# Kernel optimization log

Measured on AMD Instinct MI355X. Metric: run time of the kernel, lower is better.

The kernel has to match this reference:

```python
import jax, jax.numpy as jnp
import numpy as np

HEADS = 8
DIM_HEAD = 64
C = 512              # in_channels == inner_dim = heads*dim_head
WIN = 7              # window size implied by rel_pos table (2*7-1 = 13)
EPS = 1e-5


def setup_inputs() -> dict:
    key = jax.random.key(0)
    ks = jax.random.split(key, 6)
    B = 2048
    inner = HEADS * DIM_HEAD
    x = jax.random.normal(ks[0], (B, C, WIN, WIN), dtype=jnp.float32)
    gamma = jnp.ones((C,), dtype=jnp.float32)
    beta = jnp.zeros((C,), dtype=jnp.float32)
    w_qkv = jax.random.normal(ks[1], (C, 3 * inner), dtype=jnp.float32) / np.sqrt(C)
    rel_table = jax.random.normal(ks[2], (2 * WIN - 1, 2 * WIN - 1, HEADS), dtype=jnp.float32)
    w_out = jax.random.normal(ks[3], (inner, C), dtype=jnp.float32) / np.sqrt(inner)
    b_out = jnp.zeros((C,), dtype=jnp.float32)
    return {"x": x, "gamma": gamma, "beta": beta, "w_qkv": w_qkv,
            "rel_table": rel_table, "w_out": w_out, "b_out": b_out}


def _rel_pos_bias(rel_table, H, W):
    # Swin-style additive bias: bias[h, i, j] = table[hi-hj+H-1, wi-wj+W-1, h]
    hh = jnp.arange(H)
    ww = jnp.arange(W)
    hi = jnp.repeat(hh, W)          # [N] row index of each flattened position
    wi = jnp.tile(ww, H)            # [N] col index
    dh = hi[:, None] - hi[None, :] + (H - 1)   # [N, N]
    dw = wi[:, None] - wi[None, :] + (W - 1)   # [N, N]
    bias = rel_table[dh, dw]        # [N, N, heads]
    return jnp.transpose(bias, (2, 0, 1))      # [heads, N, N]


def reference(x, gamma, beta, w_qkv, rel_table, w_out, b_out):
    B, Cc, H, W = x.shape
    N = H * W
    shortcut = x
    xs = jnp.transpose(x.reshape(B, Cc, N), (0, 2, 1))   # [B, N, C]
    # LayerNorm over channel dim
    mu = jnp.mean(xs, axis=-1, keepdims=True)
    var = jnp.var(xs, axis=-1, keepdims=True)
    xn = (xs - mu) * jax.lax.rsqrt(var + EPS) * gamma + beta
    qkv = xn @ w_qkv                                      # [B, N, 3*inner]
    q, k, v = jnp.split(qkv, 3, axis=-1)
    def heads(t):
        return jnp.transpose(t.reshape(B, N, HEADS, DIM_HEAD), (0, 2, 1, 3))  # [B,h,N,d]
    q, k, v = heads(q), heads(k), heads(v)
    scale = DIM_HEAD ** -0.5
    dots = jnp.einsum('bhnd,bhmd->bhnm', q, k) * scale   # [B,h,N,N]
    dots = dots + _rel_pos_bias(rel_table, H, W)[None]   # add Swin-style bias
    attn = jax.nn.softmax(dots, axis=-1)
    out = jnp.einsum('bhnm,bhmd->bhnd', attn, v)         # [B,h,N,d]
    out = jnp.transpose(out, (0, 2, 1, 3)).reshape(B, N, HEADS * DIM_HEAD)
    out = out @ w_out + b_out                            # [B, N, C]
    out = jnp.transpose(out, (0, 2, 1)).reshape(B, Cc, H, W)
    return out + shortcut
```

## Files before the change

### kernel.cpp

```cpp
#include <hip/hip_runtime.h>

#define BATCH 2048
#define CH 512
#define NTOK 49
#define NHEAD 8
#define DHEAD 64

typedef __attribute__((ext_vector_type(8))) short bf16x8;
typedef __attribute__((ext_vector_type(4))) float f32x4;

__device__ __forceinline__ ushort f2bf(float f) {
  union { float f; unsigned u; } v; v.f = f;
  unsigned r = v.u + 0x7fffu + ((v.u >> 16) & 1u);
  return (ushort)(r >> 16);
}

__device__ __forceinline__ float bf2f(ushort u) {
  union { unsigned u; float f; } v; v.u = ((unsigned)u) << 16;
  return v.f;
}

#define MFMA16(a, b, c) __builtin_amdgcn_mfma_f32_16x16x32_bf16((a), (b), (c), 0, 0, 0)

#define GLOAD_LDS16(gsrc, ldst)                                                  \
  __builtin_amdgcn_global_load_lds((const __attribute__((address_space(1))) void*)(gsrc), \
                                   (__attribute__((address_space(3))) void*)(ldst), 16, 0, 0)

__global__ void prep_kernel(const float* __restrict__ w_qkv, const float* __restrict__ w_out,
                            const float* __restrict__ rel, ushort* __restrict__ wqkvB,
                            ushort* __restrict__ woutF, float* __restrict__ biasP) {
  int tid = blockIdx.x * blockDim.x + threadIdx.x;
  int stride = gridDim.x * blockDim.x;
  for (int i = tid; i < 12 * 16 * 8 * 64 * 8; i += stride) {
    int j = i & 7, lane = (i >> 3) & 63, cbs = (i >> 9) & 7, kk = (i >> 12) & 15, nb = i >> 16;
    int o = nb * 128 + cbs * 16 + (lane & 15);
    int c = kk * 32 + (lane >> 4) * 8 + j;
    wqkvB[i] = f2bf(w_qkv[c * 1536 + o]);
  }
  for (int i = tid; i < 32 * 16 * 64 * 8; i += stride) {
    int j = i & 7, lane = (i >> 3) & 63, ks = (i >> 9) & 15, cb = i >> 13;
    int o = cb * 16 + (lane & 15);
    int c = ks * 32 + (lane >> 4) * 8 + j;
    woutF[i] = f2bf(w_out[c * 512 + o]);
  }
  for (int i = tid; i < NHEAD * 64 * 64; i += stride) {
    int h = i >> 12, n = (i >> 6) & 63, m = i & 63;
    float v = -1e30f;
    if (n < NTOK && m < NTOK) {
      int dh = n / 7 - m / 7 + 6;
      int dw = n % 7 - m % 7 + 6;
      v = rel[(dh * 13 + dw) * 8 + h];
    }
    biasP[i] = v;
  }
}

__global__ __launch_bounds__(256) void ln_kernel(const float* __restrict__ x,
                                                 const float* __restrict__ gamma,
                                                 const float* __restrict__ beta,
                                                 ushort* __restrict__ xnW) {
  int b = blockIdx.x;
  int t = threadIdx.x;
  __shared__ ushort xsb[CH][NTOK];
  __shared__ float muL[64], rsL[64];
  const float4* x4 = (const float4*)(x + (size_t)b * CH * NTOK);
  for (int i4 = t; i4 < CH * NTOK / 4; i4 += 256) {
    float4 v = x4[i4];
    int lf = i4 * 4;
#pragma unroll
    for (int e = 0; e < 4; e++) {
      int idx = lf + e;
      int c = idx / NTOK, n = idx - c * NTOK;
      xsb[c][n] = f2bf(((const float*)&v)[e]);
    }
  }
  __syncthreads();
  int row = t >> 2, sub = t & 3;
  float s = 0.f, s2 = 0.f;
  if (row < NTOK) {
    for (int c = sub; c < CH; c += 4) {
      float v = bf2f(xsb[c][row]);
      s += v;
      s2 += v * v;
    }
  }
  s += __shfl_xor(s, 1);
  s += __shfl_xor(s, 2);
  s2 += __shfl_xor(s2, 1);
  s2 += __shfl_xor(s2, 2);
  if (sub == 0 && row < NTOK) {
    float m = s * (1.f / CH);
    muL[row] = m;
    rsL[row] = rsqrtf(s2 * (1.f / CH) - m * m + 1e-5f);
  }
  __syncthreads();
  ushort* dst = xnW + (size_t)b * NTOK * CH;
  for (int i = t; i < NTOK * 64; i += 256) {
    int n = i >> 6, c0 = (i & 63) * 8;
    float mu = muL[n], rs = rsL[n];
    ushort tmp[8];
#pragma unroll
    for (int j = 0; j < 8; j++) {
      int c = c0 + j;
      tmp[j] = f2bf((bf2f(xsb[c][n]) - mu) * rs * gamma[c] + beta[c]);
    }
    *(uint4*)(dst + (size_t)n * CH + c0) = *(const uint4*)tmp;
  }
}

__global__ __launch_bounds__(256, 4) void qkv_gemm(const ushort* __restrict__ xnW,
                                                   const ushort* __restrict__ wqkvB,
                                                   ushort* __restrict__ qW,
                                                   ushort* __restrict__ kW,
                                                   ushort* __restrict__ vW) {
  int bid = blockIdx.x;
  int f = (bid & 7) * 1536 + (bid >> 3);
  int mb = f / 12, nb = f - mb * 12;
  int b0 = mb * 2;
  int t = threadIdx.x, lane = t & 63, w = t >> 6;
  int wm = w >> 1, wn = w & 1;

  __shared__ __align__(16) ushort lds[8704];

  for (int i = t; i < 2 * 30 * 32; i += 256) {
    int buf = i >= 960;
    int r2 = i - buf * 960;
    int rr = r2 >> 5;
    int row = (rr < 15) ? (49 + rr) : (98 + rr);
    lds[buf * 4096 + row * 32 + (i & 31)] = 0;
  }

  const int arow = lane & 15, g = lane >> 4;
  int srow0 = w * 16 + (lane >> 2);
  int cL = lane & 3;
  const ushort* wBbase = wqkvB + (size_t)nb * 16 * 4096;

  {
#pragma unroll
    for (int i = 0; i < 2; i++) {
      int row = i * 64 + srow0;
      int n = row & 63, bb = b0 + (row >> 6);
      int cG = cL ^ ((row >> 1) & 3);
      if (n < NTOK)
        GLOAD_LDS16(xnW + ((size_t)bb * NTOK + n) * CH + cG * 8, lds + (i * 64 + w * 16) * 32);
    }
  }
  __syncthreads();

  f32x4 acc[4][4];
#pragma unroll
  for (int mt = 0; mt < 4; mt++)
#pragma unroll
    for (int nt = 0; nt < 4; nt++) acc[mt][nt] = (f32x4){0.f, 0.f, 0.f, 0.f};

  int cur = 0;
  for (int step = 0; step < 16; ++step) {
    const ushort* wp = wBbase + (size_t)step * 4096 + (wn * 4) * 512 + lane * 8;
    bf16x8 bfr[4];
#pragma unroll
    for (int nt = 0; nt < 4; nt++) bfr[nt] = *(const bf16x8*)(wp + nt * 512);
    if (step < 15) {
      int nxt = cur ^ 1, kk = step + 1;
#pragma unroll
      for (int i = 0; i < 2; i++) {
        int row = i * 64 + srow0;
        int n = row & 63, bb = b0 + (row >> 6);
        int cG = cL ^ ((row >> 1) & 3);
        if (n < NTOK)
          GLOAD_LDS16(xnW + ((size_t)bb * NTOK + n) * CH + kk * 32 + cG * 8,
                      lds + nxt * 4096 + (i * 64 + w * 16) * 32);
      }
    }
    const ushort* lA = lds + cur * 4096;
    bf16x8 afr[4];
#pragma unroll
    for (int mt = 0; mt < 4; mt++) {
      int row = wm * 64 + mt * 16 + arow;
      afr[mt] = *(const bf16x8*)&lA[row * 32 + (g ^ ((row >> 1) & 3)) * 8];
    }
#pragma unroll
    for (int mt = 0; mt < 4; mt++)
#pragma unroll
      for (int nt = 0; nt < 4; nt++) acc[mt][nt] = MFMA16(afr[mt], bfr[nt], acc[mt][nt]);
    __syncthreads();
    cur ^= 1;
  }

  ushort(*oL)[136] = (ushort(*)[136])lds;
  int h0 = (nb & 3) * 2;
  int sct = nb >> 2;
#pragma unroll
  for (int hh = 0; hh < 2; hh++) {
    if (wm == hh) {
#pragma unroll
      for (int mt = 0; mt < 4; mt++)
#pragma unroll
        for (int nt = 0; nt < 4; nt++)
#pragma unroll
          for (int r = 0; r < 4; r++) {
            int rn = mt * 16 + 4 * g + r;
            oL[rn][wn * 64 + nt * 16 + arow] = f2bf(acc[mt][nt][r]);
          }
    }
    __syncthreads();
    int b = b0 + hh;
    if (sct < 2) {
      ushort* dst = (sct == 0 ? qW : kW);
      for (int i = t; i < NTOK * 16; i += 256) {
        int n = i >> 4, c8 = i & 15;
        int h = h0 + (c8 >> 3);
        *(uint4*)(dst + (size_t)(b * 8 + h) * (NTOK * 64) + n * 64 + (c8 & 7) * 8) =
            *(const uint4*)&oL[n][c8 * 8];
      }
    } else {
      for (int i = t; i < 128 * 8; i += 256) {
        int col = i >> 3, n8 = i & 7;
        int h = h0 + (col >> 6), d = col & 63;
        ushort tmp[8];
#pragma unroll
        for (int jj = 0; jj < 8; jj++) tmp[jj] = oL[n8 * 8 + jj][col];
        *(uint4*)(vW + (size_t)(b * 8 + h) * 4096 + d * 64 + n8 * 8) = *(const uint4*)tmp;
      }
    }
    __syncthreads();
  }
}

__global__ __launch_bounds__(512, 4) void attn2(const ushort* __restrict__ qW,
                                                const ushort* __restrict__ kW,
                                                const ushort* __restrict__ vW,
                                                const float* __restrict__ biasP,
                                                ushort* __restrict__ aoW) {
  int b = blockIdx.x;
  int t = threadIdx.x;
  int lane = t & 63;
  int h = t >> 6;

  __shared__ ushort pL[8][64][72];
  ushort(*pl)[72] = pL[h];

  const int c = lane & 15, g = lane >> 4;
  const ushort* qb = qW + (size_t)(b * 8 + h) * NTOK * 64;
  const ushort* kb = kW + (size_t)(b * 8 + h) * NTOK * 64;
  const ushort* vb = vW + (size_t)(b * 8 + h) * 64 * 64;
  const float* bp = biasP + h * 64 * 64;

  f32x4 s[4][4];
#pragma unroll
  for (int mt = 0; mt < 4; mt++)
#pragma unroll
    for (int nt = 0; nt < 4; nt++) s[mt][nt] = (f32x4){0.f, 0.f, 0.f, 0.f};
#pragma unroll
  for (int ks = 0; ks < 2; ks++) {
    bf16x8 kf[4];
#pragma unroll
    for (int nt = 0; nt < 4; nt++)
      kf[nt] = *(const bf16x8*)(kb + (size_t)(nt * 16 + c) * 64 + ks * 32 + g * 8);
#pragma unroll
    for (int mt = 0; mt < 4; mt++) {
      bf16x8 qf = *(const bf16x8*)(qb + (size_t)(mt * 16 + c) * 64 + ks * 32 + g * 8);
#pragma unroll
      for (int nt = 0; nt < 4; nt++) s[mt][nt] = MFMA16(qf, kf[nt], s[mt][nt]);
    }
  }
#pragma unroll
  for (int mt = 0; mt < 4; mt++)
#pragma unroll
    for (int nt = 0; nt < 4; nt++)
#pragma unroll
      for (int r = 0; r < 4; r++) {
        int n = mt * 16 + 4 * g + r;
        int m = nt * 16 + c;
        s[mt][nt][r] = s[mt][nt][r] * 0.125f + bp[n * 64 + m];
      }

#pragma unroll
  for (int mt = 0; mt < 4; mt++)
#pragma unroll
    for (int r = 0; r < 4; r++) {
      float mx = fmaxf(fmaxf(s[mt][0][r], s[mt][1][r]), fmaxf(s[mt][2][r], s[mt][3][r]));
      mx = fmaxf(mx, __shfl_xor(mx, 1));
      mx = fmaxf(mx, __shfl_xor(mx, 2));
      mx = fmaxf(mx, __shfl_xor(mx, 4));
      mx = fmaxf(mx, __shfl_xor(mx, 8));
      float p0 = __expf(s[mt][0][r] - mx);
      float p1 = __expf(s[mt][1][r] - mx);
      float p2 = __expf(s[mt][2][r] - mx);
      float p3 = __expf(s[mt][3][r] - mx);
      float sum = p0 + p1 + p2 + p3;
      sum += __shfl_xor(sum, 1);
      sum += __shfl_xor(sum, 2);
      sum += __shfl_xor(sum, 4);
      sum += __shfl_xor(sum, 8);
      float rinv = 1.f / sum;
      int n = mt * 16 + 4 * g + r;
      pl[n][0 * 16 + c] = f2bf(p0 * rinv);
      pl[n][1 * 16 + c] = f2bf(p1 * rinv);
      pl[n][2 * 16 + c] = f2bf(p2 * rinv);
      pl[n][3 * 16 + c] = f2bf(p3 * rinv);
    }

  f32x4 o[4][4];
#pragma unroll
  for (int mt = 0; mt < 4; mt++)
#pragma unroll
    for (int nt = 0; nt < 4; nt++) o[mt][nt] = (f32x4){0.f, 0.f, 0.f, 0.f};
#pragma unroll
  for (int ks = 0; ks < 2; ks++) {
    bf16x8 vf[4];
#pragma unroll
    for (int nt = 0; nt < 4; nt++)
      vf[nt] = *(const bf16x8*)(vb + (size_t)(nt * 16 + c) * 64 + ks * 32 + g * 8);
#pragma unroll
    for (int mt = 0; mt < 4; mt++) {
      bf16x8 pf = *(const bf16x8*)&pl[mt * 16 + c][ks * 32 + g * 8];
#pragma unroll
      for (int nt = 0; nt < 4; nt++) o[mt][nt] = MFMA16(pf, vf[nt], o[mt][nt]);
    }
  }

#pragma unroll
  for (int mt = 0; mt < 4; mt++)
#pragma unroll
    for (int nt = 0; nt < 4; nt++)
#pragma unroll
      for (int r = 0; r < 4; r++) {
        int n = mt * 16 + 4 * g + r;
        pl[n][nt * 16 + c] = f2bf(o[mt][nt][r]);
      }
  ushort* ao = aoW + (size_t)b * NTOK * CH + h * 64;
  for (int i = lane; i < NTOK * 8; i += 64) {
    int row = i >> 3, c8 = i & 7;
    *(uint4*)(ao + (size_t)row * CH + c8 * 8) = *(const uint4*)&pl[row][c8 * 8];
  }
}

__global__ __launch_bounds__(256, 4) void proj_kernel(const ushort* __restrict__ aoW,
                                                      const ushort* __restrict__ woutF,
                                                      const float* __restrict__ b_out,
                                                      const float* __restrict__ x,
                                                      float* __restrict__ out) {
  int bid = blockIdx.x;
  int f = (bid & 7) * 512 + (bid >> 3);
  int mb = f >> 2, nbp = f & 3;
  int b0 = mb * 2;
  int t = threadIdx.x, lane = t & 63, w = t >> 6;
  int wm = w >> 1, wn = w & 1;

  __shared__ __align__(16) char ldsraw[33792];
  ushort* lds = (ushort*)ldsraw;
  float(*oL)[132] = (float(*)[132])ldsraw;

  for (int i = t; i < 2 * 30 * 32; i += 256) {
    int buf = i >= 960;
    int r2 = i - buf * 960;
    int rr = r2 >> 5;
    int row = (rr < 15) ? (49 + rr) : (98 + rr);
    lds[buf * 4096 + row * 32 + (i & 31)] = 0;
  }

  const int arow = lane & 15, g = lane >> 4;
  int srow0 = w * 16 + (lane >> 2);
  int cL = lane & 3;

  {
#pragma unroll
    for (int i = 0; i < 2; i++) {
      int row = i * 64 + srow0;
      int n = row & 63, bb = b0 + (row >> 6);
      int cG = cL ^ ((row >> 1) & 3);
      if (n < NTOK)
        GLOAD_LDS16(aoW + ((size_t)bb * NTOK + n) * CH + cG * 8, lds + (i * 64 + w * 16) * 32);
    }
  }
  __syncthreads();

  f32x4 acc[4][4];
#pragma unroll
  for (int mt = 0; mt < 4; mt++)
#pragma unroll
    for (int nt = 0; nt < 4; nt++) acc[mt][nt] = (f32x4){0.f, 0.f, 0.f, 0.f};

  int cur = 0;
  for (int step = 0; step < 16; ++step) {
    const ushort* wp = woutF + ((size_t)(nbp * 8 + wn * 4) * 16 + step) * 512 + lane * 8;
    bf16x8 bfr[4];
#pragma unroll
    for (int nt = 0; nt < 4; nt++) bfr[nt] = *(const bf16x8*)(wp + (size_t)nt * 16 * 512);
    if (step < 15) {
      int nxt = cur ^ 1, kk = step + 1;
#pragma unroll
      for (int i = 0; i < 2; i++) {
        int row = i * 64 + srow0;
        int n = row & 63, bb = b0 + (row >> 6);
        int cG = cL ^ ((row >> 1) & 3);
        if (n < NTOK)
          GLOAD_LDS16(aoW + ((size_t)bb * NTOK + n) * CH + kk * 32 + cG * 8,
                      lds + nxt * 4096 + (i * 64 + w * 16) * 32);
      }
    }
    const ushort* lA = lds + cur * 4096;
    bf16x8 afr[4];
#pragma unroll
    for (int mt = 0; mt < 4; mt++) {
      int row = wm * 64 + mt * 16 + arow;
      afr[mt] = *(const bf16x8*)&lA[row * 32 + (g ^ ((row >> 1) & 3)) * 8];
    }
#pragma unroll
    for (int mt = 0; mt < 4; mt++)
#pragma unroll
      for (int nt = 0; nt < 4; nt++) acc[mt][nt] = MFMA16(afr[mt], bfr[nt], acc[mt][nt]);
    __syncthreads();
    cur ^= 1;
  }

  const float* bo = b_out + nbp * 128;
#pragma unroll
  for (int hh = 0; hh < 2; hh++) {
    if (wm == hh) {
#pragma unroll
      for (int mt = 0; mt < 4; mt++)
#pragma unroll
        for (int nt = 0; nt < 4; nt++)
#pragma unroll
          for (int r = 0; r < 4; r++) {
            int rn = mt * 16 + 4 * g + r;
            if (rn < NTOK) oL[rn][wn * 64 + nt * 16 + arow] = acc[mt][nt][r];
          }
    }
    __syncthreads();
    int b = b0 + hh;
    const float4* x4 = (const float4*)(x + ((size_t)b * CH + nbp * 128) * NTOK);
    float4* o4 = (float4*)(out + ((size_t)b * CH + nbp * 128) * NTOK);
    for (int i = t; i < 1568; i += 256) {
      float4 xv = x4[i];
      float4 ov;
      int lf = i * 4;
#pragma unroll
      for (int e = 0; e < 4; e++) {
        int cl = (lf + e) / NTOK, n = (lf + e) - cl * NTOK;
        ((float*)&ov)[e] = oL[n][cl] + bo[cl] + ((const float*)&xv)[e];
      }
      o4[i] = ov;
    }
    __syncthreads();
  }
}

extern "C" void kernel_launch(void* const* d_in, const int* in_sizes, int n_in,
                              void* d_out, int out_size, void* d_ws, size_t ws_size,
                              hipStream_t stream) {
  const float* x = (const float*)d_in[0];
  const float* gamma = (const float*)d_in[1];
  const float* beta = (const float*)d_in[2];
  const float* w_qkv = (const float*)d_in[3];
  const float* rel = (const float*)d_in[4];
  const float* w_out = (const float*)d_in[5];
  const float* b_out = (const float*)d_in[6];
  float* out = (float*)d_out;

  char* ws = (char*)d_ws;
  size_t off = 0;
  ushort* wqkvB = (ushort*)(ws + off); off += (size_t)12 * 16 * 4096 * 2;
  ushort* woutF = (ushort*)(ws + off); off += (size_t)512 * 512 * 2;
  float* biasP = (float*)(ws + off);   off += (size_t)NHEAD * 64 * 64 * 4;
  ushort* qW = (ushort*)(ws + off);    off += ((size_t)BATCH * 8 * NTOK * 64 + 1024) * 2;
  ushort* kW = (ushort*)(ws + off);    off += ((size_t)BATCH * 8 * NTOK * 64 + 1024) * 2;
  ushort* vW = (ushort*)(ws + off);    off += (size_t)BATCH * 8 * 64 * 64 * 2;
  ushort* xnW = (ushort*)(ws + off);   off += (size_t)BATCH * NTOK * CH * 2;
  ushort* aoW = xnW;
  (void)ws_size;

  prep_kernel<<<1024, 256, 0, stream>>>(w_qkv, w_out, rel, wqkvB, woutF, biasP);
  ln_kernel<<<BATCH, 256, 0, stream>>>(x, gamma, beta, xnW);
  qkv_gemm<<<BATCH / 2 * 12, 256, 0, stream>>>(xnW, wqkvB, qW, kW, vW);
  attn2<<<BATCH, 512, 0, stream>>>(qW, kW, vW, biasP, aoW);
  proj_kernel<<<BATCH / 2 * 4, 256, 0, stream>>>(aoW, woutF, b_out, x, out);
}
```

Measured before the change: 640.6 us.

## Pack token rows densely in QKV GEMM instead of padding each batch to 64

```diff
diff --git a/kernel.cpp b/kernel.cpp
--- a/kernel.cpp
+++ b/kernel.cpp
@@ -114,36 +114,25 @@
                                                    ushort* __restrict__ kW,
                                                    ushort* __restrict__ vW) {
   int bid = blockIdx.x;
-  int f = (bid & 7) * 1536 + (bid >> 3);
+  int f = (bid & 7) * 1176 + (bid >> 3);
   int mb = f / 12, nb = f - mb * 12;
-  int b0 = mb * 2;
+  int r0 = mb * 128;
   int t = threadIdx.x, lane = t & 63, w = t >> 6;
   int wm = w >> 1, wn = w & 1;
 
   __shared__ __align__(16) ushort lds[8704];
-
-  for (int i = t; i < 2 * 30 * 32; i += 256) {
-    int buf = i >= 960;
-    int r2 = i - buf * 960;
-    int rr = r2 >> 5;
-    int row = (rr < 15) ? (49 + rr) : (98 + rr);
-    lds[buf * 4096 + row * 32 + (i & 31)] = 0;
-  }
 
   const int arow = lane & 15, g = lane >> 4;
   int srow0 = w * 16 + (lane >> 2);
   int cL = lane & 3;
   const ushort* wBbase = wqkvB + (size_t)nb * 16 * 4096;
-
-  {
-#pragma unroll
-    for (int i = 0; i < 2; i++) {
-      int row = i * 64 + srow0;
-      int n = row & 63, bb = b0 + (row >> 6);
-      int cG = cL ^ ((row >> 1) & 3);
-      if (n < NTOK)
-        GLOAD_LDS16(xnW + ((size_t)bb * NTOK + n) * CH + cG * 8, lds + (i * 64 + w * 16) * 32);
-    }
+  const ushort* xbase = xnW + (size_t)r0 * CH;
+
+#pragma unroll
+  for (int i = 0; i < 2; i++) {
+    int row = i * 64 + srow0;
+    int cG = cL ^ ((row >> 1) & 3);
+    GLOAD_LDS16(xbase + (size_t)row * CH + cG * 8, lds + (i * 64 + w * 16) * 32);
   }
   __syncthreads();
 
@@ -164,11 +153,9 @@
 #pragma unroll
       for (int i = 0; i < 2; i++) {
         int row = i * 64 + srow0;
-        int n = row & 63, bb = b0 + (row >> 6);
         int cG = cL ^ ((row >> 1) & 3);
-        if (n < NTOK)
-          GLOAD_LDS16(xnW + ((size_t)bb * NTOK + n) * CH + kk * 32 + cG * 8,
-                      lds + nxt * 4096 + (i * 64 + w * 16) * 32);
+        GLOAD_LDS16(xbase + (size_t)row * CH + kk * 32 + cG * 8,
+                    lds + nxt * 4096 + (i * 64 + w * 16) * 32);
       }
     }
     const ushort* lA = lds + cur * 4096;
@@ -203,23 +190,23 @@
           }
     }
     __syncthreads();
-    int b = b0 + hh;
     if (sct < 2) {
       ushort* dst = (sct == 0 ? qW : kW);
-      for (int i = t; i < NTOK * 16; i += 256) {
-        int n = i >> 4, c8 = i & 15;
+      for (int i = t; i < 64 * 16; i += 256) {
+        int rn = i >> 4, c8 = i & 15;
+        int grow = r0 + hh * 64 + rn;
+        int b = grow / 49, n = grow - b * 49;
         int h = h0 + (c8 >> 3);
         *(uint4*)(dst + (size_t)(b * 8 + h) * (NTOK * 64) + n * 64 + (c8 & 7) * 8) =
-            *(const uint4*)&oL[n][c8 * 8];
+            *(const uint4*)&oL[rn][c8 * 8];
       }
     } else {
-      for (int i = t; i < 128 * 8; i += 256) {
-        int col = i >> 3, n8 = i & 7;
+      for (int i = t; i < 64 * 128; i += 256) {
+        int rn = i & 63, col = i >> 6;
+        int grow = r0 + hh * 64 + rn;
+        int b = grow / 49, n = grow - b * 49;
         int h = h0 + (col >> 6), d = col & 63;
-        ushort tmp[8];
-#pragma unroll
-        for (int jj = 0; jj < 8; jj++) tmp[jj] = oL[n8 * 8 + jj][col];
-        *(uint4*)(vW + (size_t)(b * 8 + h) * 4096 + d * 64 + n8 * 8) = *(const uint4*)tmp;
+        vW[(size_t)(b * 8 + h) * 4096 + d * 64 + n] = oL[rn][col];
       }
     }
     __syncthreads();
@@ -473,7 +460,7 @@
 
   prep_kernel<<<1024, 256, 0, stream>>>(w_qkv, w_out, rel, wqkvB, woutF, biasP);
   ln_kernel<<<BATCH, 256, 0, stream>>>(x, gamma, beta, xnW);
-  qkv_gemm<<<BATCH / 2 * 12, 256, 0, stream>>>(xnW, wqkvB, qW, kW, vW);
+  qkv_gemm<<<784 * 12, 256, 0, stream>>>(xnW, wqkvB, qW, kW, vW);
   attn2<<<BATCH, 512, 0, stream>>>(qW, kW, vW, biasP, aoW);
   proj_kernel<<<BATCH / 2 * 4, 256, 0, stream>>>(aoW, woutF, b_out, x, out);
 }
```

After: 617.9 us. 3.5% less time.
